# Kernel tuning notes

Hardware: AMD Instinct MI355X
Metric: run time of the kernel (lower is better)

Reference implementation:

```python
import jax, jax.numpy as jnp
import numpy as np

D_MODEL, D_K, D_V, N_HEADS = 1024, 64, 64, 16
BATCH, N_CTX = 2, 2048


def half_causal_allowed(n):
    # rows [0, n/2): attend to cols [0, n/2) only (dense block)
    # rows [n/2, n): standard causal (col <= row)
    i = jnp.arange(n)[:, None]
    j = jnp.arange(n)[None, :]
    top = (i < n // 2) & (j < n // 2)
    bot = (i >= n // 2) & (j <= i)
    return top | bot  # [n, n] bool


def setup_inputs() -> dict:
    key = jax.random.key(0)
    ks = jax.random.split(key, 8)
    s_in = 1.0 / np.sqrt(D_MODEL)
    s_out = 1.0 / np.sqrt(D_V * N_HEADS)
    return {
        "x": jax.random.normal(ks[0], (BATCH, N_CTX, D_MODEL), jnp.float32),
        # Linear weights stored [in, out] (transpose of torch layout)
        "Wq": jax.random.uniform(ks[1], (D_MODEL, D_K * N_HEADS), jnp.float32, -s_in, s_in),
        "bq": jax.random.uniform(ks[2], (D_K * N_HEADS,), jnp.float32, -s_in, s_in),
        "Wk": jax.random.uniform(ks[3], (D_MODEL, D_K * N_HEADS), jnp.float32, -s_in, s_in),
        "bk": jax.random.uniform(ks[4], (D_K * N_HEADS,), jnp.float32, -s_in, s_in),
        "Wv": jax.random.uniform(ks[5], (D_MODEL, D_V * N_HEADS), jnp.float32, -s_in, s_in),
        "bv": jax.random.uniform(ks[6], (D_V * N_HEADS,), jnp.float32, -s_in, s_in),
        "Wo": jax.random.uniform(ks[7], (D_V * N_HEADS, D_MODEL), jnp.float32, -s_out, s_out),
    }


def reference(x, Wq, bq, Wk, bk, Wv, bv, Wo):
    b, n, _ = x.shape
    h, dk, dv = N_HEADS, D_K, D_V
    # projections -> [b, h, n, d]
    q = (x @ Wq + bq).reshape(b, n, h, dk).transpose(0, 2, 1, 3)
    k = (x @ Wk + bk).reshape(b, n, h, dk).transpose(0, 2, 1, 3)
    v = (x @ Wv + bv).reshape(b, n, h, dv).transpose(0, 2, 1, 3)
    scores = jnp.einsum("bhqd,bhkd->bhqk", q / jnp.sqrt(jnp.float32(dk)), k)
    allowed = half_causal_allowed(n)  # [n, n]
    scores = jnp.where(allowed, scores, -jnp.inf)
    attn = jax.nn.softmax(scores, axis=-1)  # dropout p=0 -> identity
    out = jnp.einsum("bhqk,bhkd->bhqd", attn, v)
    out = out.transpose(0, 2, 1, 3).reshape(b, n, h * dv)
    return out @ Wo  # final Linear has no bias
```

## Files before the change

### kernel.cpp

```cpp
#include <hip/hip_runtime.h>
#include <hip/hip_bf16.h>

#define NH 16
#define DH 64
#define DM 1024
#define NC 2048
#define MROWS 4096
#define KVT 64

#define SCALE_Q 0.180336880f

typedef __attribute__((ext_vector_type(8))) short short8;
typedef __attribute__((ext_vector_type(4))) float f32x4;
typedef __attribute__((ext_vector_type(16))) float f32x16;
typedef __attribute__((ext_vector_type(4))) unsigned int uint4e;

__device__ __forceinline__ unsigned pkbf16(float a, float b) {
    unsigned r;
    asm("v_cvt_pk_bf16_f32 %0, %1, %2" : "=v"(r) : "v"(a), "v"(b));
    return r;
}
__device__ __forceinline__ unsigned short f2bf(float x) {
    return (unsigned short)(pkbf16(x, x) & 0xffffu);
}
__device__ __forceinline__ float exp2v(float x) {
    float r;
    asm("v_exp_f32 %0, %1" : "=v"(r) : "v"(x));
    return r;
}
__device__ __forceinline__ f32x16 fzero16() {
    f32x16 r;
    #pragma unroll
    for (int i = 0; i < 16; ++i) r[i] = 0.f;
    return r;
}
__device__ __forceinline__ short8 mk8(unsigned w0, unsigned w1, unsigned w2, unsigned w3) {
    uint4e u = {w0, w1, w2, w3};
    return __builtin_bit_cast(short8, u);
}
__device__ __forceinline__ void gload16(const unsigned short* g, unsigned short* l) {
    __builtin_amdgcn_global_load_lds(
        (const __attribute__((address_space(1))) void*)g,
        (__attribute__((address_space(3))) void*)l, 16, 0, 0);
}

__global__ __launch_bounds__(256) void cvt_x(const float* __restrict__ in,
                                             unsigned short* __restrict__ out, int n8)
{
    int i = blockIdx.x * 256 + threadIdx.x;
    if (i >= n8) return;
    const float4 a = ((const float4*)in)[i * 2];
    const float4 b = ((const float4*)in)[i * 2 + 1];
    uint4e u = {pkbf16(a.x, a.y), pkbf16(a.z, a.w), pkbf16(b.x, b.y), pkbf16(b.z, b.w)};
    ((uint4e*)out)[i] = u;
}

__global__ __launch_bounds__(256) void cvt_w4(const float* __restrict__ W0,
                                              const float* __restrict__ W1,
                                              const float* __restrict__ W2,
                                              const float* __restrict__ W3,
                                              unsigned short* __restrict__ Wt4)
{
    __shared__ unsigned short T[64][72];
    const int z = blockIdx.z;
    const float* W = (z == 0) ? W0 : (z == 1) ? W1 : (z == 2) ? W2 : W3;
    unsigned short* Wt = Wt4 + (size_t)z * DM * DM;
    const int t = threadIdx.x;
    const int r = t >> 2, s = t & 3;
    const int bi = blockIdx.y;
    const int bj = blockIdx.x;
    const float* src = W + (size_t)(bi * 64 + r) * DM + bj * 64 + s * 16;
    float4 f0 = ((const float4*)src)[0];
    float4 f1 = ((const float4*)src)[1];
    float4 f2 = ((const float4*)src)[2];
    float4 f3 = ((const float4*)src)[3];
    uint2 u;
    u.x = pkbf16(f0.x, f0.y); u.y = pkbf16(f0.z, f0.w); *(uint2*)&T[r][s * 16]      = u;
    u.x = pkbf16(f1.x, f1.y); u.y = pkbf16(f1.z, f1.w); *(uint2*)&T[r][s * 16 + 4]  = u;
    u.x = pkbf16(f2.x, f2.y); u.y = pkbf16(f2.z, f2.w); *(uint2*)&T[r][s * 16 + 8]  = u;
    u.x = pkbf16(f3.x, f3.y); u.y = pkbf16(f3.z, f3.w); *(uint2*)&T[r][s * 16 + 12] = u;
    __syncthreads();
    unsigned short vals[16];
    #pragma unroll
    for (int j = 0; j < 16; ++j) vals[j] = T[s * 16 + j][r];
    unsigned short* dst = Wt + (size_t)(bj * 64 + r) * DM + bi * 64 + s * 16;
    *(short8*)(dst)     = *(short8*)&vals[0];
    *(short8*)(dst + 8) = *(short8*)&vals[8];
}

__global__ __launch_bounds__(256) void gemm_qkv(const unsigned short* __restrict__ A,
                                                const unsigned short* __restrict__ Bt,
                                                const float* __restrict__ bq,
                                                const float* __restrict__ bk,
                                                const float* __restrict__ bv,
                                                unsigned short* __restrict__ Out)
{
    __shared__ unsigned short As[128 * 32];
    __shared__ unsigned short Bs[128 * 32];
    const int t  = threadIdx.x;
    const int w  = t >> 6, l = t & 63;
    const int wr = w >> 1, wc = w & 1;
    const int m0 = blockIdx.y << 7;
    const int n0 = blockIdx.x << 7;

    f32x4 acc[4][4] = {};
    const int nkt = DM >> 5;
    for (int kt = 0; kt < nkt; ++kt) {
        #pragma unroll
        for (int j = 0; j < 2; ++j) {
            const int c0 = j * 256 + w * 64;
            const int cc = c0 + l;
            const int row = cc >> 2, qq = cc & 3;
            gload16(A  + (size_t)(m0 + row) * DM + kt * 32 + qq * 8, &As[c0 * 8]);
            gload16(Bt + (size_t)(n0 + row) * DM + kt * 32 + qq * 8, &Bs[c0 * 8]);
        }
        __syncthreads();
        short8 af[4], bf_[4];
        #pragma unroll
        for (int mi = 0; mi < 4; ++mi)
            af[mi] = *(short8*)&As[(wr * 64 + mi * 16 + (l & 15)) * 32 + (l >> 4) * 8];
        #pragma unroll
        for (int ni = 0; ni < 4; ++ni)
            bf_[ni] = *(short8*)&Bs[(wc * 64 + ni * 16 + (l & 15)) * 32 + (l >> 4) * 8];
        #pragma unroll
        for (int mi = 0; mi < 4; ++mi)
            #pragma unroll
            for (int ni = 0; ni < 4; ++ni)
                acc[mi][ni] = __builtin_amdgcn_mfma_f32_16x16x32_bf16(
                                  af[mi], bf_[ni], acc[mi][ni], 0, 0, 0);
        __syncthreads();
    }

    const int seg = n0 >> 10;
    const float* bias = (seg == 0) ? bq : (seg == 1) ? bk : bv;
    const float scale = (seg == 0) ? SCALE_Q : 1.0f;
    unsigned short* C = Out + (size_t)seg * MROWS * DM;
    const int ncol0 = (n0 & 1023) + wc * 64;
    float bvv[4];
    #pragma unroll
    for (int ni = 0; ni < 4; ++ni)
        bvv[ni] = bias[ncol0 + ni * 16 + (l & 15)];
    #pragma unroll
    for (int mi = 0; mi < 4; ++mi)
        #pragma unroll
        for (int ni = 0; ni < 4; ++ni) {
            const int gcol = ncol0 + ni * 16 + (l & 15);
            #pragma unroll
            for (int r = 0; r < 4; ++r) {
                const int grow = m0 + wr * 64 + mi * 16 + (l >> 4) * 4 + r;
                C[(size_t)grow * DM + gcol] = f2bf((acc[mi][ni][r] + bvv[ni]) * scale);
            }
        }
}

__global__ __launch_bounds__(256) void gemm_wo(const unsigned short* __restrict__ A,
                                               const unsigned short* __restrict__ Bt,
                                               float* __restrict__ C)
{
    __shared__ unsigned short As[64 * 32];
    __shared__ unsigned short Bs[128 * 32];
    const int t = threadIdx.x, w = t >> 6, l = t & 63;
    const int wr = w >> 1, wc = w & 1;
    const int m0 = blockIdx.y << 6;
    const int n0 = blockIdx.x << 7;

    f32x4 acc[2][4] = {};
    const int nkt = DM >> 5;
    for (int kt = 0; kt < nkt; ++kt) {
        {
            const int c0 = w * 64;
            const int cc = c0 + l;
            const int row = cc >> 2, qq = cc & 3;
            gload16(A + (size_t)(m0 + row) * DM + kt * 32 + qq * 8, &As[c0 * 8]);
        }
        #pragma unroll
        for (int j = 0; j < 2; ++j) {
            const int c0 = j * 256 + w * 64;
            const int cc = c0 + l;
            const int row = cc >> 2, qq = cc & 3;
            gload16(Bt + (size_t)(n0 + row) * DM + kt * 32 + qq * 8, &Bs[c0 * 8]);
        }
        __syncthreads();
        short8 af[2], bf_[4];
        #pragma unroll
        for (int mi = 0; mi < 2; ++mi)
            af[mi] = *(short8*)&As[(wr * 32 + mi * 16 + (l & 15)) * 32 + (l >> 4) * 8];
        #pragma unroll
        for (int ni = 0; ni < 4; ++ni)
            bf_[ni] = *(short8*)&Bs[(wc * 64 + ni * 16 + (l & 15)) * 32 + (l >> 4) * 8];
        #pragma unroll
        for (int mi = 0; mi < 2; ++mi)
            #pragma unroll
            for (int ni = 0; ni < 4; ++ni)
                acc[mi][ni] = __builtin_amdgcn_mfma_f32_16x16x32_bf16(
                                  af[mi], bf_[ni], acc[mi][ni], 0, 0, 0);
        __syncthreads();
    }
    #pragma unroll
    for (int mi = 0; mi < 2; ++mi)
        #pragma unroll
        for (int ni = 0; ni < 4; ++ni) {
            const int gcol = n0 + wc * 64 + ni * 16 + (l & 15);
            #pragma unroll
            for (int r = 0; r < 4; ++r) {
                const int grow = m0 + wr * 32 + mi * 16 + (l >> 4) * 4 + r;
                C[(size_t)grow * DM + gcol] = acc[mi][ni][r];
            }
        }
}

__global__ __launch_bounds__(128) void attn_mfma(const unsigned short* __restrict__ Qg,
                                                 const unsigned short* __restrict__ Kg,
                                                 const unsigned short* __restrict__ Vg,
                                                 unsigned short* __restrict__ Og)
{
    __shared__ unsigned short Ks[2][64][68];
    __shared__ unsigned short Vt[2][64][68];
    const int t   = threadIdx.x;
    const int w   = t >> 6;
    const int l   = t & 63;
    const int l31 = l & 31;
    const int hi  = l >> 5;

    const int f   = blockIdx.x;
    const int xcd = f & 7;
    const int pos = f >> 3;
    const int bh  = xcd * 4 + (pos >> 5);
    int qt = pos & 31;
    if ((pos >> 5) & 1) qt = 31 - qt;
    const int b = bh >> 4;
    const int h = bh & 15;

    const int qb = qt << 6;
    const int wq = qb + w * 32;
    const size_t rb0 = (size_t)b * NC;
    const int hd = h * DH;

    const unsigned short* qp = Qg + (rb0 + wq + l31) * DM + hd + hi * 8;
    short8 fq[4];
    #pragma unroll
    for (int c = 0; c < 4; ++c)
        fq[c] = *(const short8*)(qp + c * 16);

    f32x16 o0 = fzero16(), o1 = fzero16();
    float mrun = -1e30f, lrun = 0.f;
    const bool bottom = (qb >= NC / 2);
    const int nkv = bottom ? (qt + 1) : 16;
    const int srow = t >> 1;
    const int sseg = t & 1;

    short8 kr[4], vr[4];
    auto loadKV = [&](int kbase) {
        const unsigned short* kp = Kg + (rb0 + kbase + srow) * DM + hd + sseg * 32;
        const unsigned short* vp = Vg + (rb0 + kbase + srow) * DM + hd + sseg * 32;
        #pragma unroll
        for (int i = 0; i < 4; ++i) {
            kr[i] = *(const short8*)(kp + i * 8);
            vr[i] = *(const short8*)(vp + i * 8);
        }
    };
    auto writeKV = [&](int bufi) {
        #pragma unroll
        for (int i = 0; i < 4; ++i) {
            uint4e ku = __builtin_bit_cast(uint4e, kr[i]);
            uint2 u01; u01.x = ku.x; u01.y = ku.y;
            uint2 u23; u23.x = ku.z; u23.y = ku.w;
            *(uint2*)&Ks[bufi][srow][sseg * 32 + i * 8]     = u01;
            *(uint2*)&Ks[bufi][srow][sseg * 32 + i * 8 + 4] = u23;
            #pragma unroll
            for (int j = 0; j < 8; ++j)
                Vt[bufi][sseg * 32 + i * 8 + j][srow] = (unsigned short)vr[i][j];
        }
    };

    loadKV(0);
    writeKV(0);

    for (int it = 0; it < nkv; ++it) {
        __syncthreads();
        const int kb = it * KVT;
        const int cur = it & 1;
        const bool havenext = (it + 1 < nkv);
        if (havenext) loadKV((it + 1) * KVT);

        const bool active = bottom ? (kb <= wq + 31) : true;
        if (active) {
            f32x16 s0 = fzero16(), s1 = fzero16();
            #pragma unroll
            for (int c = 0; c < 4; ++c) {
                const int off = c * 16 + hi * 8;
                uint2 a0 = *(const uint2*)&Ks[cur][l31][off];
                uint2 a1 = *(const uint2*)&Ks[cur][l31][off + 4];
                uint2 b0 = *(const uint2*)&Ks[cur][32 + l31][off];
                uint2 b1 = *(const uint2*)&Ks[cur][32 + l31][off + 4];
                s0 = __builtin_amdgcn_mfma_f32_32x32x16_bf16(
                        mk8(a0.x, a0.y, a1.x, a1.y), fq[c], s0, 0, 0, 0);
                s1 = __builtin_amdgcn_mfma_f32_32x32x16_bf16(
                        mk8(b0.x, b0.y, b1.x, b1.y), fq[c], s1, 0, 0, 0);
            }
            if (bottom && (kb + KVT - 1 > wq)) {
                const int qg = wq + l31;
                #pragma unroll
                for (int r = 0; r < 16; ++r) {
                    const int kk = (r & 3) + 8 * (r >> 2) + 4 * hi;
                    if (kb + kk > qg)      s0[r] = -1e30f;
                    if (kb + 32 + kk > qg) s1[r] = -1e30f;
                }
            }
            float tm[16];
            #pragma unroll
            for (int r = 0; r < 16; ++r) tm[r] = fmaxf(s0[r], s1[r]);
            #pragma unroll
            for (int st = 8; st > 0; st >>= 1)
                #pragma unroll
                for (int r = 0; r < 8; ++r)
                    if (r < st) tm[r] = fmaxf(tm[r], tm[r + st]);
            float pm = fmaxf(tm[0], __shfl_xor(tm[0], 32));
            if (!__all(pm - mrun <= 8.f)) {
                const float mnew = fmaxf(mrun, pm);
                const float corr = exp2v(mrun - mnew);
                mrun = mnew;
                lrun *= corr;
                #pragma unroll
                for (int i = 0; i < 16; ++i) { o0[i] *= corr; o1[i] *= corr; }
            }
            float rs = 0.f;
            #pragma unroll
            for (int r = 0; r < 16; ++r) { s0[r] = exp2v(s0[r] - mrun); rs += s0[r]; }
            #pragma unroll
            for (int r = 0; r < 16; ++r) { s1[r] = exp2v(s1[r] - mrun); rs += s1[r]; }
            rs += __shfl_xor(rs, 32);
            lrun += rs;
            #pragma unroll
            for (int kc = 0; kc < 4; ++kc) {
                const f32x16 src = (kc < 2) ? s0 : s1;
                const int rbase = (kc & 1) * 8;
                unsigned A01 = pkbf16(src[rbase + 0], src[rbase + 1]);
                unsigned A23 = pkbf16(src[rbase + 2], src[rbase + 3]);
                unsigned A45 = pkbf16(src[rbase + 4], src[rbase + 5]);
                unsigned A67 = pkbf16(src[rbase + 6], src[rbase + 7]);
                unsigned s01 = (unsigned)__shfl_xor((int)A01, 32);
                unsigned s23 = (unsigned)__shfl_xor((int)A23, 32);
                unsigned s45 = (unsigned)__shfl_xor((int)A45, 32);
                unsigned s67 = (unsigned)__shfl_xor((int)A67, 32);
                short8 fp = hi ? mk8(s45, s67, A45, A67)
                               : mk8(A01, A23, s01, s23);
                const int voff = kc * 16 + hi * 8;
                uint2 va0 = *(const uint2*)&Vt[cur][l31][voff];
                uint2 va1 = *(const uint2*)&Vt[cur][l31][voff + 4];
                uint2 vb0 = *(const uint2*)&Vt[cur][32 + l31][voff];
                uint2 vb1 = *(const uint2*)&Vt[cur][32 + l31][voff + 4];
                o0 = __builtin_amdgcn_mfma_f32_32x32x16_bf16(
                        mk8(va0.x, va0.y, va1.x, va1.y), fp, o0, 0, 0, 0);
                o1 = __builtin_amdgcn_mfma_f32_32x32x16_bf16(
                        mk8(vb0.x, vb0.y, vb1.x, vb1.y), fp, o1, 0, 0, 0);
            }
        }
        if (havenext) writeKV((it + 1) & 1);
    }
    __syncthreads();

    const float inv = 1.f / lrun;
    unsigned short* obuf = (unsigned short*)&Ks[0][0][0];
    {
        unsigned short* reg = obuf + (size_t)(w * 32 + l31) * 72;
        #pragma unroll
        for (int r = 0; r < 16; ++r) {
            const int dd = (r & 3) + 8 * (r >> 2) + 4 * hi;
            reg[dd]      = f2bf(o0[r] * inv);
            reg[dd + 32] = f2bf(o1[r] * inv);
        }
    }
    __syncthreads();
    {
        const int row = t >> 1, seg = t & 1;
        const unsigned short* src = obuf + (size_t)row * 72 + seg * 32;
        unsigned short* dst = Og + (rb0 + qb + row) * DM + hd + seg * 32;
        #pragma unroll
        for (int i = 0; i < 4; ++i)
            *(short8*)(dst + i * 8) = *(const short8*)(src + i * 8);
    }
}

extern "C" void kernel_launch(void* const* d_in, const int* in_sizes, int n_in,
                              void* d_out, int out_size, void* d_ws, size_t ws_size,
                              hipStream_t stream)
{
    const float* x  = (const float*)d_in[0];
    const float* Wq = (const float*)d_in[1];
    const float* bq = (const float*)d_in[2];
    const float* Wk = (const float*)d_in[3];
    const float* bk = (const float*)d_in[4];
    const float* Wv = (const float*)d_in[5];
    const float* bv = (const float*)d_in[6];
    const float* Wo = (const float*)d_in[7];
    float* out = (float*)d_out;

    char* ws = (char*)d_ws;
    const size_t szA = (size_t)MROWS * DM * 2;
    const size_t szW = (size_t)DM * DM * 2;
    unsigned short* xb  = (unsigned short*)(ws);
    unsigned short* wqT = (unsigned short*)(ws + szA);
    unsigned short* woT = (unsigned short*)(ws + szA + 3 * szW);
    unsigned short* qb_ = (unsigned short*)(ws + szA + 4 * szW);
    unsigned short* kb_ = (unsigned short*)(ws + 2 * szA + 4 * szW);
    unsigned short* vb_ = (unsigned short*)(ws + 3 * szA + 4 * szW);
    unsigned short* ab_ = (unsigned short*)(ws + 4 * szA + 4 * szW);

    cvt_x<<<dim3(MROWS * DM / 8 / 256), 256, 0, stream>>>(x, xb, MROWS * DM / 8);
    cvt_w4<<<dim3(16, 16, 4), 256, 0, stream>>>(Wq, Wk, Wv, Wo, wqT);

    gemm_qkv<<<dim3(24, 32), 256, 0, stream>>>(xb, wqT, bq, bk, bv, qb_);
    attn_mfma<<<dim3(1024), 128, 0, stream>>>(qb_, kb_, vb_, ab_);
    gemm_wo<<<dim3(8, 64), 256, 0, stream>>>(ab_, woT, out);
}
```

Baseline: 135.3 us.

## Replace LDS-staged attention with register-direct single-wave kernel and pre-transposed V

Adds a kernel that transposes V into a per-head [d, n] layout, reusing the x-bf16 workspace. The attention kernel becomes one wave per 32-query tile: K and transposed V fragments are loaded straight from global memory into MFMA operand registers. This removes LDS staging, the scalar V transpose and block barriers, and K loads for the next tile are prefetched into registers. It also adds s_setprio around the MFMA phases. The cost is an extra launch and pass over V, plus uncoalesced strided global loads that rely on L2 reuse, and twice as many blocks.

New measurement: 158.5 us. 1.17x slower.

```diff
diff --git a/kernel.cpp b/kernel.cpp
--- a/kernel.cpp
+++ b/kernel.cpp
@@ -88,6 +88,28 @@
     *(short8*)(dst + 8) = *(short8*)&vals[8];
 }
 
+__global__ __launch_bounds__(256) void cvt_vT(const unsigned short* __restrict__ V,
+                                              unsigned short* __restrict__ Vt)
+{
+    __shared__ unsigned short T[64][72];
+    const int t  = threadIdx.x;
+    const int nx = blockIdx.x;
+    const int bh = blockIdx.y;
+    const int b  = bh >> 4, h = bh & 15;
+    const int n0 = nx << 6;
+    const int r  = t >> 2, s = t & 3;
+    const unsigned short* src = V + ((size_t)b * NC + n0 + r) * DM + h * 64 + s * 16;
+    *(short8*)&T[r][s * 16]     = *(const short8*)(src);
+    *(short8*)&T[r][s * 16 + 8] = *(const short8*)(src + 8);
+    __syncthreads();
+    unsigned short vals[16];
+    #pragma unroll
+    for (int j = 0; j < 16; ++j) vals[j] = T[s * 16 + j][r];
+    unsigned short* dst = Vt + ((size_t)bh * 64 + r) * NC + n0 + s * 16;
+    *(short8*)(dst)     = *(short8*)&vals[0];
+    *(short8*)(dst + 8) = *(short8*)&vals[8];
+}
+
 __global__ __launch_bounds__(256) void gemm_qkv(const unsigned short* __restrict__ A,
                                                 const unsigned short* __restrict__ Bt,
                                                 const float* __restrict__ bq,
@@ -209,34 +231,33 @@
         }
 }
 
-__global__ __launch_bounds__(128) void attn_mfma(const unsigned short* __restrict__ Qg,
-                                                 const unsigned short* __restrict__ Kg,
-                                                 const unsigned short* __restrict__ Vg,
-                                                 unsigned short* __restrict__ Og)
-{
-    __shared__ unsigned short Ks[2][64][68];
-    __shared__ unsigned short Vt[2][64][68];
-    const int t   = threadIdx.x;
-    const int w   = t >> 6;
-    const int l   = t & 63;
+__global__ __launch_bounds__(64, 2) void attn_reg(const unsigned short* __restrict__ Qg,
+                                                  const unsigned short* __restrict__ Kg,
+                                                  const unsigned short* __restrict__ Vtg,
+                                                  unsigned short* __restrict__ Og)
+{
+    __shared__ unsigned short ob[32][72];
+    const int l   = threadIdx.x;
     const int l31 = l & 31;
     const int hi  = l >> 5;
 
     const int f   = blockIdx.x;
     const int xcd = f & 7;
     const int pos = f >> 3;
-    const int bh  = xcd * 4 + (pos >> 5);
-    int qt = pos & 31;
-    if ((pos >> 5) & 1) qt = 31 - qt;
+    const int bh  = xcd * 4 + (pos >> 6);
+    int qt = pos & 63;
+    if ((pos >> 6) & 1) qt = 63 - qt;
     const int b = bh >> 4;
     const int h = bh & 15;
 
-    const int qb = qt << 6;
-    const int wq = qb + w * 32;
+    const int qb = qt << 5;
     const size_t rb0 = (size_t)b * NC;
     const int hd = h * DH;
 
-    const unsigned short* qp = Qg + (rb0 + wq + l31) * DM + hd + hi * 8;
+    const unsigned short* Kbase = Kg + rb0 * DM + hd;
+    const unsigned short* Vbase = Vtg + (size_t)bh * 64 * NC;
+
+    const unsigned short* qp = Qg + (rb0 + qb + l31) * DM + hd + hi * 8;
     short8 fq[4];
     #pragma unroll
     for (int c = 0; c < 4; ++c)
@@ -245,125 +266,105 @@
     f32x16 o0 = fzero16(), o1 = fzero16();
     float mrun = -1e30f, lrun = 0.f;
     const bool bottom = (qb >= NC / 2);
-    const int nkv = bottom ? (qt + 1) : 16;
-    const int srow = t >> 1;
-    const int sseg = t & 1;
-
-    short8 kr[4], vr[4];
-    auto loadKV = [&](int kbase) {
-        const unsigned short* kp = Kg + (rb0 + kbase + srow) * DM + hd + sseg * 32;
-        const unsigned short* vp = Vg + (rb0 + kbase + srow) * DM + hd + sseg * 32;
-        #pragma unroll
-        for (int i = 0; i < 4; ++i) {
-            kr[i] = *(const short8*)(kp + i * 8);
-            vr[i] = *(const short8*)(vp + i * 8);
-        }
-    };
-    auto writeKV = [&](int bufi) {
-        #pragma unroll
-        for (int i = 0; i < 4; ++i) {
-            uint4e ku = __builtin_bit_cast(uint4e, kr[i]);
-            uint2 u01; u01.x = ku.x; u01.y = ku.y;
-            uint2 u23; u23.x = ku.z; u23.y = ku.w;
-            *(uint2*)&Ks[bufi][srow][sseg * 32 + i * 8]     = u01;
-            *(uint2*)&Ks[bufi][srow][sseg * 32 + i * 8 + 4] = u23;
-            #pragma unroll
-            for (int j = 0; j < 8; ++j)
-                Vt[bufi][sseg * 32 + i * 8 + j][srow] = (unsigned short)vr[i][j];
-        }
-    };
-
-    loadKV(0);
-    writeKV(0);
+    const int nkv = bottom ? ((qt + 2) >> 1) : 16;
+
+    short8 kA[4], kB[4];
+    {
+        const unsigned short* ka = Kbase + (size_t)(l31) * DM + hi * 8;
+        const unsigned short* kb_ = Kbase + (size_t)(32 + l31) * DM + hi * 8;
+        #pragma unroll
+        for (int c = 0; c < 4; ++c) {
+            kA[c] = *(const short8*)(ka + c * 16);
+            kB[c] = *(const short8*)(kb_ + c * 16);
+        }
+    }
 
     for (int it = 0; it < nkv; ++it) {
-        __syncthreads();
         const int kb = it * KVT;
-        const int cur = it & 1;
-        const bool havenext = (it + 1 < nkv);
-        if (havenext) loadKV((it + 1) * KVT);
-
-        const bool active = bottom ? (kb <= wq + 31) : true;
-        if (active) {
-            f32x16 s0 = fzero16(), s1 = fzero16();
+        short8 vA[4], vB[4];
+        {
+            const unsigned short* va = Vbase + (size_t)l31 * NC + kb + hi * 8;
+            const unsigned short* vb = Vbase + (size_t)(32 + l31) * NC + kb + hi * 8;
             #pragma unroll
             for (int c = 0; c < 4; ++c) {
-                const int off = c * 16 + hi * 8;
-                uint2 a0 = *(const uint2*)&Ks[cur][l31][off];
-                uint2 a1 = *(const uint2*)&Ks[cur][l31][off + 4];
-                uint2 b0 = *(const uint2*)&Ks[cur][32 + l31][off];
-                uint2 b1 = *(const uint2*)&Ks[cur][32 + l31][off + 4];
-                s0 = __builtin_amdgcn_mfma_f32_32x32x16_bf16(
-                        mk8(a0.x, a0.y, a1.x, a1.y), fq[c], s0, 0, 0, 0);
-                s1 = __builtin_amdgcn_mfma_f32_32x32x16_bf16(
-                        mk8(b0.x, b0.y, b1.x, b1.y), fq[c], s1, 0, 0, 0);
+                vA[c] = *(const short8*)(va + c * 16);
+                vB[c] = *(const short8*)(vb + c * 16);
             }
-            if (bottom && (kb + KVT - 1 > wq)) {
-                const int qg = wq + l31;
-                #pragma unroll
-                for (int r = 0; r < 16; ++r) {
-                    const int kk = (r & 3) + 8 * (r >> 2) + 4 * hi;
-                    if (kb + kk > qg)      s0[r] = -1e30f;
-                    if (kb + 32 + kk > qg) s1[r] = -1e30f;
-                }
+        }
+        f32x16 s0 = fzero16(), s1 = fzero16();
+        __builtin_amdgcn_s_setprio(1);
+        #pragma unroll
+        for (int c = 0; c < 4; ++c) {
+            s0 = __builtin_amdgcn_mfma_f32_32x32x16_bf16(kA[c], fq[c], s0, 0, 0, 0);
+            s1 = __builtin_amdgcn_mfma_f32_32x32x16_bf16(kB[c], fq[c], s1, 0, 0, 0);
+        }
+        __builtin_amdgcn_s_setprio(0);
+        if (it + 1 < nkv) {
+            const unsigned short* ka = Kbase + (size_t)((it + 1) * KVT + l31) * DM + hi * 8;
+            const unsigned short* kb2 = Kbase + (size_t)((it + 1) * KVT + 32 + l31) * DM + hi * 8;
+            #pragma unroll
+            for (int c = 0; c < 4; ++c) {
+                kA[c] = *(const short8*)(ka + c * 16);
+                kB[c] = *(const short8*)(kb2 + c * 16);
             }
-            float tm[16];
-            #pragma unroll
-            for (int r = 0; r < 16; ++r) tm[r] = fmaxf(s0[r], s1[r]);
-            #pragma unroll
-            for (int st = 8; st > 0; st >>= 1)
-                #pragma unroll
-                for (int r = 0; r < 8; ++r)
-                    if (r < st) tm[r] = fmaxf(tm[r], tm[r + st]);
-            float pm = fmaxf(tm[0], __shfl_xor(tm[0], 32));
-            if (!__all(pm - mrun <= 8.f)) {
-                const float mnew = fmaxf(mrun, pm);
-                const float corr = exp2v(mrun - mnew);
-                mrun = mnew;
-                lrun *= corr;
-                #pragma unroll
-                for (int i = 0; i < 16; ++i) { o0[i] *= corr; o1[i] *= corr; }
+        }
+        if (bottom && (kb + KVT - 1 > qb)) {
+            const int qg = qb + l31;
+            #pragma unroll
+            for (int r = 0; r < 16; ++r) {
+                const int kk = (r & 3) + 8 * (r >> 2) + 4 * hi;
+                if (kb + kk > qg)      s0[r] = -1e30f;
+                if (kb + 32 + kk > qg) s1[r] = -1e30f;
             }
-            float rs = 0.f;
-            #pragma unroll
-            for (int r = 0; r < 16; ++r) { s0[r] = exp2v(s0[r] - mrun); rs += s0[r]; }
-            #pragma unroll
-            for (int r = 0; r < 16; ++r) { s1[r] = exp2v(s1[r] - mrun); rs += s1[r]; }
-            rs += __shfl_xor(rs, 32);
-            lrun += rs;
-            #pragma unroll
-            for (int kc = 0; kc < 4; ++kc) {
-                const f32x16 src = (kc < 2) ? s0 : s1;
-                const int rbase = (kc & 1) * 8;
-                unsigned A01 = pkbf16(src[rbase + 0], src[rbase + 1]);
-                unsigned A23 = pkbf16(src[rbase + 2], src[rbase + 3]);
-                unsigned A45 = pkbf16(src[rbase + 4], src[rbase + 5]);
-                unsigned A67 = pkbf16(src[rbase + 6], src[rbase + 7]);
-                unsigned s01 = (unsigned)__shfl_xor((int)A01, 32);
-                unsigned s23 = (unsigned)__shfl_xor((int)A23, 32);
-                unsigned s45 = (unsigned)__shfl_xor((int)A45, 32);
-                unsigned s67 = (unsigned)__shfl_xor((int)A67, 32);
-                short8 fp = hi ? mk8(s45, s67, A45, A67)
-                               : mk8(A01, A23, s01, s23);
-                const int voff = kc * 16 + hi * 8;
-                uint2 va0 = *(const uint2*)&Vt[cur][l31][voff];
-                uint2 va1 = *(const uint2*)&Vt[cur][l31][voff + 4];
-                uint2 vb0 = *(const uint2*)&Vt[cur][32 + l31][voff];
-                uint2 vb1 = *(const uint2*)&Vt[cur][32 + l31][voff + 4];
-                o0 = __builtin_amdgcn_mfma_f32_32x32x16_bf16(
-                        mk8(va0.x, va0.y, va1.x, va1.y), fp, o0, 0, 0, 0);
-                o1 = __builtin_amdgcn_mfma_f32_32x32x16_bf16(
-                        mk8(vb0.x, vb0.y, vb1.x, vb1.y), fp, o1, 0, 0, 0);
-            }
-        }
-        if (havenext) writeKV((it + 1) & 1);
-    }
-    __syncthreads();
+        }
+        float tm[16];
+        #pragma unroll
+        for (int r = 0; r < 16; ++r) tm[r] = fmaxf(s0[r], s1[r]);
+        #pragma unroll
+        for (int st = 8; st > 0; st >>= 1)
+            #pragma unroll
+            for (int r = 0; r < 8; ++r)
+                if (r < st) tm[r] = fmaxf(tm[r], tm[r + st]);
+        float pm = fmaxf(tm[0], __shfl_xor(tm[0], 32));
+        if (!__all(pm - mrun <= 8.f)) {
+            const float mnew = fmaxf(mrun, pm);
+            const float corr = exp2v(mrun - mnew);
+            mrun = mnew;
+            lrun *= corr;
+            #pragma unroll
+            for (int i = 0; i < 16; ++i) { o0[i] *= corr; o1[i] *= corr; }
+        }
+        float rs = 0.f;
+        #pragma unroll
+        for (int r = 0; r < 16; ++r) { s0[r] = exp2v(s0[r] - mrun); rs += s0[r]; }
+        #pragma unroll
+        for (int r = 0; r < 16; ++r) { s1[r] = exp2v(s1[r] - mrun); rs += s1[r]; }
+        rs += __shfl_xor(rs, 32);
+        lrun += rs;
+        __builtin_amdgcn_s_setprio(1);
+        #pragma unroll
+        for (int kc = 0; kc < 4; ++kc) {
+            const f32x16 src = (kc < 2) ? s0 : s1;
+            const int rbase = (kc & 1) * 8;
+            unsigned A01 = pkbf16(src[rbase + 0], src[rbase + 1]);
+            unsigned A23 = pkbf16(src[rbase + 2], src[rbase + 3]);
+            unsigned A45 = pkbf16(src[rbase + 4], src[rbase + 5]);
+            unsigned A67 = pkbf16(src[rbase + 6], src[rbase + 7]);
+            unsigned s01 = (unsigned)__shfl_xor((int)A01, 32);
+            unsigned s23 = (unsigned)__shfl_xor((int)A23, 32);
+            unsigned s45 = (unsigned)__shfl_xor((int)A45, 32);
+            unsigned s67 = (unsigned)__shfl_xor((int)A67, 32);
+            short8 fp = hi ? mk8(s45, s67, A45, A67)
+                           : mk8(A01, A23, s01, s23);
+            o0 = __builtin_amdgcn_mfma_f32_32x32x16_bf16(vA[kc], fp, o0, 0, 0, 0);
+            o1 = __builtin_amdgcn_mfma_f32_32x32x16_bf16(vB[kc], fp, o1, 0, 0, 0);
+        }
+        __builtin_amdgcn_s_setprio(0);
+    }
 
     const float inv = 1.f / lrun;
-    unsigned short* obuf = (unsigned short*)&Ks[0][0][0];
     {
-        unsigned short* reg = obuf + (size_t)(w * 32 + l31) * 72;
+        unsigned short* reg = &ob[l31][0];
         #pragma unroll
         for (int r = 0; r < 16; ++r) {
             const int dd = (r & 3) + 8 * (r >> 2) + 4 * hi;
@@ -371,10 +372,9 @@
             reg[dd + 32] = f2bf(o1[r] * inv);
         }
     }
-    __syncthreads();
     {
-        const int row = t >> 1, seg = t & 1;
-        const unsigned short* src = obuf + (size_t)row * 72 + seg * 32;
+        const int row = l >> 1, seg = l & 1;
+        const unsigned short* src = &ob[row][seg * 32];
         unsigned short* dst = Og + (rb0 + qb + row) * DM + hd + seg * 32;
         #pragma unroll
         for (int i = 0; i < 4; ++i)
@@ -406,11 +406,13 @@
     unsigned short* kb_ = (unsigned short*)(ws + 2 * szA + 4 * szW);
     unsigned short* vb_ = (unsigned short*)(ws + 3 * szA + 4 * szW);
     unsigned short* ab_ = (unsigned short*)(ws + 4 * szA + 4 * szW);
+    unsigned short* vt_ = xb;
 
     cvt_x<<<dim3(MROWS * DM / 8 / 256), 256, 0, stream>>>(x, xb, MROWS * DM / 8);
     cvt_w4<<<dim3(16, 16, 4), 256, 0, stream>>>(Wq, Wk, Wv, Wo, wqT);
 
     gemm_qkv<<<dim3(24, 32), 256, 0, stream>>>(xb, wqT, bq, bk, bv, qb_);
-    attn_mfma<<<dim3(1024), 128, 0, stream>>>(qb_, kb_, vb_, ab_);
+    cvt_vT<<<dim3(32, 32), 256, 0, stream>>>(vb_, vt_);
+    attn_reg<<<dim3(2048), 64, 0, stream>>>(qb_, kb_, vt_, ab_);
     gemm_wo<<<dim3(8, 64), 256, 0, stream>>>(ab_, woT, out);
 }
```

## Store V pre-transposed and stage K/V via async direct-to-LDS loads with swizzle

Applied to the files above, without the earlier changes.

The QKV GEMM epilogue now writes V in a per-head transposed [b,h,d,n] layout, so the attention kernel no longer transposes V element by element in LDS. K and V tiles are loaded straight into LDS with 16-byte global-to-LDS loads using an XOR swizzle, which replaces the register staging and the padded arrays. The inner loop also drops the per-wave active check, raises wave priority around the MFMA blocks and sets a min-blocks launch bound. In exchange, the transposed V stores from the GEMM are strided, uncoalesced 2-byte writes, which could slow that epilogue.

Measured after the change: 124.0 us. 8.3% less time.

```diff
diff --git a/kernel.cpp b/kernel.cpp
--- a/kernel.cpp
+++ b/kernel.cpp
@@ -134,23 +134,42 @@
     const int seg = n0 >> 10;
     const float* bias = (seg == 0) ? bq : (seg == 1) ? bk : bv;
     const float scale = (seg == 0) ? SCALE_Q : 1.0f;
-    unsigned short* C = Out + (size_t)seg * MROWS * DM;
     const int ncol0 = (n0 & 1023) + wc * 64;
     float bvv[4];
     #pragma unroll
     for (int ni = 0; ni < 4; ++ni)
         bvv[ni] = bias[ncol0 + ni * 16 + (l & 15)];
-    #pragma unroll
-    for (int mi = 0; mi < 4; ++mi)
-        #pragma unroll
-        for (int ni = 0; ni < 4; ++ni) {
-            const int gcol = ncol0 + ni * 16 + (l & 15);
-            #pragma unroll
-            for (int r = 0; r < 4; ++r) {
-                const int grow = m0 + wr * 64 + mi * 16 + (l >> 4) * 4 + r;
-                C[(size_t)grow * DM + gcol] = f2bf((acc[mi][ni][r] + bvv[ni]) * scale);
+
+    if (seg == 2) {
+        unsigned short* vt = Out + 2 * (size_t)MROWS * DM;
+        #pragma unroll
+        for (int mi = 0; mi < 4; ++mi)
+            #pragma unroll
+            for (int ni = 0; ni < 4; ++ni) {
+                const int gcol = ncol0 + ni * 16 + (l & 15);
+                const int h_ = gcol >> 6, d_ = gcol & 63;
+                #pragma unroll
+                for (int r = 0; r < 4; ++r) {
+                    const int grow = m0 + wr * 64 + mi * 16 + (l >> 4) * 4 + r;
+                    const int b_ = grow >> 11, n_ = grow & 2047;
+                    vt[(((size_t)b_ * 16 + h_) * 64 + d_) * NC + n_] =
+                        f2bf(acc[mi][ni][r] + bvv[ni]);
+                }
             }
-        }
+    } else {
+        unsigned short* C = Out + (size_t)seg * MROWS * DM;
+        #pragma unroll
+        for (int mi = 0; mi < 4; ++mi)
+            #pragma unroll
+            for (int ni = 0; ni < 4; ++ni) {
+                const int gcol = ncol0 + ni * 16 + (l & 15);
+                #pragma unroll
+                for (int r = 0; r < 4; ++r) {
+                    const int grow = m0 + wr * 64 + mi * 16 + (l >> 4) * 4 + r;
+                    C[(size_t)grow * DM + gcol] = f2bf((acc[mi][ni][r] + bvv[ni]) * scale);
+                }
+            }
+    }
 }
 
 __global__ __launch_bounds__(256) void gemm_wo(const unsigned short* __restrict__ A,
@@ -209,13 +228,13 @@
         }
 }
 
-__global__ __launch_bounds__(128) void attn_mfma(const unsigned short* __restrict__ Qg,
-                                                 const unsigned short* __restrict__ Kg,
-                                                 const unsigned short* __restrict__ Vg,
-                                                 unsigned short* __restrict__ Og)
-{
-    __shared__ unsigned short Ks[2][64][68];
-    __shared__ unsigned short Vt[2][64][68];
+__global__ __launch_bounds__(128, 2) void attn_lds(const unsigned short* __restrict__ Qg,
+                                                   const unsigned short* __restrict__ Kg,
+                                                   const unsigned short* __restrict__ Vtg,
+                                                   unsigned short* __restrict__ Og)
+{
+    __shared__ unsigned short KS[2][4096];
+    __shared__ unsigned short VS[2][4096];
     const int t   = threadIdx.x;
     const int w   = t >> 6;
     const int l   = t & 63;
@@ -246,122 +265,115 @@
     float mrun = -1e30f, lrun = 0.f;
     const bool bottom = (qb >= NC / 2);
     const int nkv = bottom ? (qt + 1) : 16;
-    const int srow = t >> 1;
-    const int sseg = t & 1;
-
-    short8 kr[4], vr[4];
-    auto loadKV = [&](int kbase) {
-        const unsigned short* kp = Kg + (rb0 + kbase + srow) * DM + hd + sseg * 32;
-        const unsigned short* vp = Vg + (rb0 + kbase + srow) * DM + hd + sseg * 32;
-        #pragma unroll
-        for (int i = 0; i < 4; ++i) {
-            kr[i] = *(const short8*)(kp + i * 8);
-            vr[i] = *(const short8*)(vp + i * 8);
+
+    const unsigned short* Vbase = Vtg + (size_t)bh * 64 * NC;
+
+    auto stage = [&](int it, int buf) {
+        const int kb = it * KVT;
+        #pragma unroll
+        for (int j = 0; j < 4; ++j) {
+            const int jj  = w * 4 + j;
+            const int p   = jj * 64 + l;
+            const int row = p >> 3;
+            const int slot = (p & 7) ^ (row & 7);
+            gload16(Kg + (size_t)(rb0 + kb + row) * DM + hd + slot * 8,
+                    &KS[buf][jj * 512]);
+            gload16(Vbase + (size_t)row * NC + kb + slot * 8,
+                    &VS[buf][jj * 512]);
         }
     };
-    auto writeKV = [&](int bufi) {
-        #pragma unroll
-        for (int i = 0; i < 4; ++i) {
-            uint4e ku = __builtin_bit_cast(uint4e, kr[i]);
-            uint2 u01; u01.x = ku.x; u01.y = ku.y;
-            uint2 u23; u23.x = ku.z; u23.y = ku.w;
-            *(uint2*)&Ks[bufi][srow][sseg * 32 + i * 8]     = u01;
-            *(uint2*)&Ks[bufi][srow][sseg * 32 + i * 8 + 4] = u23;
-            #pragma unroll
-            for (int j = 0; j < 8; ++j)
-                Vt[bufi][sseg * 32 + i * 8 + j][srow] = (unsigned short)vr[i][j];
-        }
-    };
-
-    loadKV(0);
-    writeKV(0);
+
+    stage(0, 0);
+    __syncthreads();
 
     for (int it = 0; it < nkv; ++it) {
-        __syncthreads();
         const int kb = it * KVT;
         const int cur = it & 1;
-        const bool havenext = (it + 1 < nkv);
-        if (havenext) loadKV((it + 1) * KVT);
-
-        const bool active = bottom ? (kb <= wq + 31) : true;
-        if (active) {
-            f32x16 s0 = fzero16(), s1 = fzero16();
+        if (it + 1 < nkv) stage(it + 1, cur ^ 1);
+
+        const unsigned short* Kb = &KS[cur][0];
+        short8 kf[2][4];
+        #pragma unroll
+        for (int half = 0; half < 2; ++half) {
+            const int row = half * 32 + l31;
+            const int rx  = row & 7;
             #pragma unroll
             for (int c = 0; c < 4; ++c) {
-                const int off = c * 16 + hi * 8;
-                uint2 a0 = *(const uint2*)&Ks[cur][l31][off];
-                uint2 a1 = *(const uint2*)&Ks[cur][l31][off + 4];
-                uint2 b0 = *(const uint2*)&Ks[cur][32 + l31][off];
-                uint2 b1 = *(const uint2*)&Ks[cur][32 + l31][off + 4];
-                s0 = __builtin_amdgcn_mfma_f32_32x32x16_bf16(
-                        mk8(a0.x, a0.y, a1.x, a1.y), fq[c], s0, 0, 0, 0);
-                s1 = __builtin_amdgcn_mfma_f32_32x32x16_bf16(
-                        mk8(b0.x, b0.y, b1.x, b1.y), fq[c], s1, 0, 0, 0);
+                const int slot = (c * 2 + hi) ^ rx;
+                kf[half][c] = *(const short8*)(Kb + row * 64 + slot * 8);
             }
-            if (bottom && (kb + KVT - 1 > wq)) {
-                const int qg = wq + l31;
-                #pragma unroll
-                for (int r = 0; r < 16; ++r) {
-                    const int kk = (r & 3) + 8 * (r >> 2) + 4 * hi;
-                    if (kb + kk > qg)      s0[r] = -1e30f;
-                    if (kb + 32 + kk > qg) s1[r] = -1e30f;
-                }
+        }
+        f32x16 s0 = fzero16(), s1 = fzero16();
+        __builtin_amdgcn_s_setprio(1);
+        #pragma unroll
+        for (int c = 0; c < 4; ++c) {
+            s0 = __builtin_amdgcn_mfma_f32_32x32x16_bf16(kf[0][c], fq[c], s0, 0, 0, 0);
+            s1 = __builtin_amdgcn_mfma_f32_32x32x16_bf16(kf[1][c], fq[c], s1, 0, 0, 0);
+        }
+        __builtin_amdgcn_s_setprio(0);
+        if (bottom && (kb + KVT - 1 > wq)) {
+            const int qg = wq + l31;
+            #pragma unroll
+            for (int r = 0; r < 16; ++r) {
+                const int kk = (r & 3) + 8 * (r >> 2) + 4 * hi;
+                if (kb + kk > qg)      s0[r] = -1e30f;
+                if (kb + 32 + kk > qg) s1[r] = -1e30f;
             }
-            float tm[16];
-            #pragma unroll
-            for (int r = 0; r < 16; ++r) tm[r] = fmaxf(s0[r], s1[r]);
-            #pragma unroll
-            for (int st = 8; st > 0; st >>= 1)
-                #pragma unroll
-                for (int r = 0; r < 8; ++r)
-                    if (r < st) tm[r] = fmaxf(tm[r], tm[r + st]);
-            float pm = fmaxf(tm[0], __shfl_xor(tm[0], 32));
-            if (!__all(pm - mrun <= 8.f)) {
-                const float mnew = fmaxf(mrun, pm);
-                const float corr = exp2v(mrun - mnew);
-                mrun = mnew;
-                lrun *= corr;
-                #pragma unroll
-                for (int i = 0; i < 16; ++i) { o0[i] *= corr; o1[i] *= corr; }
-            }
-            float rs = 0.f;
-            #pragma unroll
-            for (int r = 0; r < 16; ++r) { s0[r] = exp2v(s0[r] - mrun); rs += s0[r]; }
-            #pragma unroll
-            for (int r = 0; r < 16; ++r) { s1[r] = exp2v(s1[r] - mrun); rs += s1[r]; }
-            rs += __shfl_xor(rs, 32);
-            lrun += rs;
-            #pragma unroll
-            for (int kc = 0; kc < 4; ++kc) {
-                const f32x16 src = (kc < 2) ? s0 : s1;
-                const int rbase = (kc & 1) * 8;
-                unsigned A01 = pkbf16(src[rbase + 0], src[rbase + 1]);
-                unsigned A23 = pkbf16(src[rbase + 2], src[rbase + 3]);
-                unsigned A45 = pkbf16(src[rbase + 4], src[rbase + 5]);
-                unsigned A67 = pkbf16(src[rbase + 6], src[rbase + 7]);
-                unsigned s01 = (unsigned)__shfl_xor((int)A01, 32);
-                unsigned s23 = (unsigned)__shfl_xor((int)A23, 32);
-                unsigned s45 = (unsigned)__shfl_xor((int)A45, 32);
-                unsigned s67 = (unsigned)__shfl_xor((int)A67, 32);
-                short8 fp = hi ? mk8(s45, s67, A45, A67)
-                               : mk8(A01, A23, s01, s23);
-                const int voff = kc * 16 + hi * 8;
-                uint2 va0 = *(const uint2*)&Vt[cur][l31][voff];
-                uint2 va1 = *(const uint2*)&Vt[cur][l31][voff + 4];
-                uint2 vb0 = *(const uint2*)&Vt[cur][32 + l31][voff];
-                uint2 vb1 = *(const uint2*)&Vt[cur][32 + l31][voff + 4];
-                o0 = __builtin_amdgcn_mfma_f32_32x32x16_bf16(
-                        mk8(va0.x, va0.y, va1.x, va1.y), fp, o0, 0, 0, 0);
-                o1 = __builtin_amdgcn_mfma_f32_32x32x16_bf16(
-                        mk8(vb0.x, vb0.y, vb1.x, vb1.y), fp, o1, 0, 0, 0);
-            }
-        }
-        if (havenext) writeKV((it + 1) & 1);
-    }
-    __syncthreads();
+        }
+        float tm[16];
+        #pragma unroll
+        for (int r = 0; r < 16; ++r) tm[r] = fmaxf(s0[r], s1[r]);
+        #pragma unroll
+        for (int st = 8; st > 0; st >>= 1)
+            #pragma unroll
+            for (int r = 0; r < 8; ++r)
+                if (r < st) tm[r] = fmaxf(tm[r], tm[r + st]);
+        float pm = fmaxf(tm[0], __shfl_xor(tm[0], 32));
+        if (!__all(pm - mrun <= 8.f)) {
+            const float mnew = fmaxf(mrun, pm);
+            const float corr = exp2v(mrun - mnew);
+            mrun = mnew;
+            lrun *= corr;
+            #pragma unroll
+            for (int i = 0; i < 16; ++i) { o0[i] *= corr; o1[i] *= corr; }
+        }
+        float rs = 0.f;
+        #pragma unroll
+        for (int r = 0; r < 16; ++r) { s0[r] = exp2v(s0[r] - mrun); rs += s0[r]; }
+        #pragma unroll
+        for (int r = 0; r < 16; ++r) { s1[r] = exp2v(s1[r] - mrun); rs += s1[r]; }
+        rs += __shfl_xor(rs, 32);
+        lrun += rs;
+        const unsigned short* Vb = &VS[cur][0];
+        __builtin_amdgcn_s_setprio(1);
+        #pragma unroll
+        for (int kc = 0; kc < 4; ++kc) {
+            const f32x16 src = (kc < 2) ? s0 : s1;
+            const int rbase = (kc & 1) * 8;
+            unsigned A01 = pkbf16(src[rbase + 0], src[rbase + 1]);
+            unsigned A23 = pkbf16(src[rbase + 2], src[rbase + 3]);
+            unsigned A45 = pkbf16(src[rbase + 4], src[rbase + 5]);
+            unsigned A67 = pkbf16(src[rbase + 6], src[rbase + 7]);
+            unsigned s01 = (unsigned)__shfl_xor((int)A01, 32);
+            unsigned s23 = (unsigned)__shfl_xor((int)A23, 32);
+            unsigned s45 = (unsigned)__shfl_xor((int)A45, 32);
+            unsigned s67 = (unsigned)__shfl_xor((int)A67, 32);
+            short8 fp = hi ? mk8(s45, s67, A45, A67)
+                           : mk8(A01, A23, s01, s23);
+            const int slot = (kc * 2 + hi);
+            const int r0_ = l31, r1_ = 32 + l31;
+            short8 v0 = *(const short8*)(Vb + r0_ * 64 + (slot ^ (r0_ & 7)) * 8);
+            short8 v1 = *(const short8*)(Vb + r1_ * 64 + (slot ^ (r1_ & 7)) * 8);
+            o0 = __builtin_amdgcn_mfma_f32_32x32x16_bf16(v0, fp, o0, 0, 0, 0);
+            o1 = __builtin_amdgcn_mfma_f32_32x32x16_bf16(v1, fp, o1, 0, 0, 0);
+        }
+        __builtin_amdgcn_s_setprio(0);
+
+        __syncthreads();
+    }
 
     const float inv = 1.f / lrun;
-    unsigned short* obuf = (unsigned short*)&Ks[0][0][0];
+    unsigned short* obuf = (unsigned short*)&KS[0][0];
     {
         unsigned short* reg = obuf + (size_t)(w * 32 + l31) * 72;
         #pragma unroll
@@ -404,13 +416,13 @@
     unsigned short* woT = (unsigned short*)(ws + szA + 3 * szW);
     unsigned short* qb_ = (unsigned short*)(ws + szA + 4 * szW);
     unsigned short* kb_ = (unsigned short*)(ws + 2 * szA + 4 * szW);
-    unsigned short* vb_ = (unsigned short*)(ws + 3 * szA + 4 * szW);
+    unsigned short* vt_ = (unsigned short*)(ws + 3 * szA + 4 * szW);
     unsigned short* ab_ = (unsigned short*)(ws + 4 * szA + 4 * szW);
 
     cvt_x<<<dim3(MROWS * DM / 8 / 256), 256, 0, stream>>>(x, xb, MROWS * DM / 8);
     cvt_w4<<<dim3(16, 16, 4), 256, 0, stream>>>(Wq, Wk, Wv, Wo, wqT);
 
     gemm_qkv<<<dim3(24, 32), 256, 0, stream>>>(xb, wqT, bq, bk, bv, qb_);
-    attn_mfma<<<dim3(1024), 128, 0, stream>>>(qb_, kb_, vb_, ab_);
+    attn_lds<<<dim3(1024), 128, 0, stream>>>(qb_, kb_, vt_, ab_);
     gemm_wo<<<dim3(8, 64), 256, 0, stream>>>(ab_, woT, out);
 }
```
